# Performance work log

Hardware: AMD Instinct MI355X
Metric: run time of the kernel (lower is better)

Reference implementation:

```python
import jax, jax.numpy as jnp
import numpy as np

DIM = 32
B, H, W = 4, 256, 256


def conv1x1(x, w, b):
    # x: [B,C,H,W], w: [O,C], b: [O]
    return jnp.einsum('bchw,oc->bohw', x, w) + b[None, :, None, None]


def conv3x3(x, w, b):
    # x: [B,C,H,W], w: [O,C,3,3]
    out = jax.lax.conv_general_dilated(
        x, w, window_strides=(1, 1), padding='SAME',
        dimension_numbers=('NCHW', 'OIHW', 'NCHW'))
    return out + b[None, :, None, None]


def fft2d(x):
    # fft2 over last two dims, then fftshift over ALL dims (torch default)
    f = jnp.fft.fftshift(jnp.fft.fft2(x, norm='ortho'))
    return jnp.concatenate([f.real, f.imag], axis=1)  # [B,2C,H,W]


def ifft2d(x):
    f = jnp.fft.ifftshift(x)  # over ALL dims (torch default)
    re, im = jnp.split(f, 2, axis=1)
    c = jax.lax.complex(re, im)
    return jnp.abs(jnp.fft.ifft2(c, norm='ortho'))  # [B,C,H,W]


def setup_inputs() -> dict:
    key = jax.random.key(0)
    ks = jax.random.split(key, 16)
    C = DIM
    s = 0.02  # small init keeps the global-HW dot products in a sane softmax range
    inp = {
        'x': jax.random.normal(ks[0], (B, C, H, W), jnp.float32),
        'y': jax.random.normal(ks[1], (B, C, H, W), jnp.float32),
        'wq': jax.random.normal(ks[2], (C, C), jnp.float32) * s,
        'bq': jnp.zeros((C,), jnp.float32),
        'wk': jax.random.normal(ks[3], (C, C), jnp.float32) * s,
        'bk': jnp.zeros((C,), jnp.float32),
        'wv': jax.random.normal(ks[4], (C, C), jnp.float32) * s,
        'bv': jnp.zeros((C,), jnp.float32),
        'wd': jax.random.normal(ks[5], (C, C), jnp.float32) * s,
        'bd': jnp.zeros((C,), jnp.float32),
        'wc': jax.random.normal(ks[6], (2 * C, 2 * C, 3, 3), jnp.float32) * s,
        'bc': jnp.zeros((2 * C,), jnp.float32),
        'wi': jax.random.normal(ks[7], (2 * C, 2 * C, 3, 3), jnp.float32) * s,
        'bi': jnp.zeros((2 * C,), jnp.float32),
    }
    return inp


def reference(x, y, wq, bq, wk, bk, wv, bv, wd, bd, wc, bc, wi, bi):
    b, c, h, w = x.shape
    xq = conv1x1(x, wq, bq).reshape(b, c, h * w)            # [B,C,HW]
    dft = conv3x3(fft2d(conv1x1(y, wd, bd)), wc, bc)        # [B,2C,H,W]
    yk, yv = jnp.split(dft, 2, axis=1)
    yk = conv1x1(yk, wk, bk).reshape(b, c, h * w)
    yv = conv1x1(yv, wv, bv).reshape(b, c, h * w)
    att = jnp.einsum('bcn,bdn->bcd', xq, yk)                # [B,C,C]
    att = jax.nn.softmax(att, axis=1)                       # softmax over dim=1 (as in torch)
    out = jnp.einsum('bcd,bdn->bcn', att, yv).reshape(b, c, h, w)
    out = out + ifft2d(conv3x3(jax.nn.relu(dft), wi, bi))
    return out
```

## Files before the change

### kernel.cpp

```cpp
#include <hip/hip_runtime.h>
#include <math.h>

#define HW_ (256*256)
#define CH 32
#define CH2 64
#define BATCH 4

typedef short bf16x8 __attribute__((ext_vector_type(8)));
typedef float f32x4 __attribute__((ext_vector_type(4)));

__device__ __forceinline__ unsigned short f2bf(float f) {
    union { float f; unsigned u; } v; v.f = f;
    unsigned r = v.u + 0x7fffu + ((v.u >> 16) & 1u);
    return (unsigned short)(r >> 16);
}
__device__ __forceinline__ float bf2f(unsigned h) {
    union { unsigned u; float f; } v; v.u = h << 16;
    return v.f;
}

__device__ __forceinline__ int ctof_slot(int s) {
    return s < 16 ? s + 16 : s < 32 ? s + 32 : s < 48 ? s - 32 : s - 16;
}

__device__ __forceinline__ float2 cmul(float2 a, float2 b) {
    return make_float2(a.x*b.x - a.y*b.y, a.x*b.y + a.y*b.x);
}

__device__ __forceinline__ uint4 relu_bf16x8(uint4 v) {
    unsigned* pv = (unsigned*)&v;
    #pragma unroll
    for (int q = 0; q < 4; ++q) {
        unsigned a = pv[q];
        unsigned lo = a & 0xffffu, hi = a >> 16;
        if (lo & 0x8000u) lo = 0;
        if (hi & 0x8000u) hi = 0;
        pv[q] = lo | (hi << 16);
    }
    return v;
}

__device__ __forceinline__ void build_tw4(float2* tw, float sign) {
    int tid = threadIdx.x;
    float ang = sign * 6.2831853071795864769f * (float)tid / 256.0f;
    float s, c; sincosf(ang, &s, &c);
    tw[tid] = make_float2(c, s);
}

template<int SGN>
__device__ __forceinline__ void fft16_reg(float2* x, const float2* tw) {
    float2 u[16];
    #pragma unroll
    for (int m0 = 0; m0 < 4; ++m0) {
        float2 x0 = x[m0], x1 = x[m0+4], x2 = x[m0+8], x3 = x[m0+12];
        float2 t0 = make_float2(x0.x+x2.x, x0.y+x2.y);
        float2 t1 = make_float2(x0.x-x2.x, x0.y-x2.y);
        float2 t2 = make_float2(x1.x+x3.x, x1.y+x3.y);
        float2 t3 = make_float2(x1.x-x3.x, x1.y-x3.y);
        float2 r  = make_float2(-SGN*t3.y, SGN*t3.x);
        u[m0*4+0] = make_float2(t0.x+t2.x, t0.y+t2.y);
        u[m0*4+1] = make_float2(t1.x+r.x,  t1.y+r.y);
        u[m0*4+2] = make_float2(t0.x-t2.x, t0.y-t2.y);
        u[m0*4+3] = make_float2(t1.x-r.x,  t1.y-r.y);
    }
    #pragma unroll
    for (int m0 = 1; m0 < 4; ++m0)
        #pragma unroll
        for (int a = 1; a < 4; ++a)
            u[m0*4+a] = cmul(u[m0*4+a], tw[(16*m0*a) & 255]);
    #pragma unroll
    for (int a = 0; a < 4; ++a) {
        float2 x0 = u[a], x1 = u[4+a], x2 = u[8+a], x3 = u[12+a];
        float2 t0 = make_float2(x0.x+x2.x, x0.y+x2.y);
        float2 t1 = make_float2(x0.x-x2.x, x0.y-x2.y);
        float2 t2 = make_float2(x1.x+x3.x, x1.y+x3.y);
        float2 t3 = make_float2(x1.x-x3.x, x1.y-x3.y);
        float2 r  = make_float2(-SGN*t3.y, SGN*t3.x);
        x[a]    = make_float2(t0.x+t2.x, t0.y+t2.y);
        x[a+4]  = make_float2(t1.x+r.x,  t1.y+r.y);
        x[a+8]  = make_float2(t0.x-t2.x, t0.y-t2.y);
        x[a+12] = make_float2(t1.x-r.x,  t1.y-r.y);
    }
}

template<int SGN>
__device__ __forceinline__ void fft_core16(float2* A, const float2* tw) {
    const int tid = threadIdx.x;
    const int l = tid >> 4;
    const int d = tid & 15;
    const int base = l*257;
    float2 x[16];
    #pragma unroll
    for (int n1 = 0; n1 < 16; ++n1) x[n1] = A[base + n1*16 + d];
    fft16_reg<SGN>(x, tw);
    #pragma unroll
    for (int k0 = 1; k0 < 16; ++k0) x[k0] = cmul(x[k0], tw[d*k0]);
    #pragma unroll
    for (int k0 = 0; k0 < 16; ++k0) A[base + k0*16 + ((d + k0) & 15)] = x[k0];
    __syncthreads();
    #pragma unroll
    for (int n0 = 0; n0 < 16; ++n0) x[n0] = A[base + d*16 + ((n0 + d) & 15)];
    fft16_reg<SGN>(x, tw);
    #pragma unroll
    for (int k1 = 0; k1 < 16; ++k1) A[base + d + k1*16] = x[k1];
    __syncthreads();
}

__global__ __launch_bounds__(256) void k_fft_fwd1(const unsigned short* __restrict__ yd, ushort2* __restrict__ CAt) {
    __shared__ float2 A[16*257];
    __shared__ float2 tw[256];
    build_tw4(tw, -1.0f);
    int blk = blockIdx.x;
    int bc = blk >> 4, h0 = (blk & 15) << 4;
    const float sc = 1.0f/16.0f;
    const unsigned short* src = yd + (size_t)bc*HW_ + (size_t)h0*256;
    for (int idx = threadIdx.x; idx < 16*64; idx += 256) {
        int l = idx >> 6, w4 = (idx & 63) << 2;
        uint2 v = *(const uint2*)(src + l*256 + w4);
        A[l*257 + w4+0] = make_float2(bf2f(v.x & 0xffffu)*sc, 0.0f);
        A[l*257 + w4+1] = make_float2(bf2f(v.x >> 16)*sc, 0.0f);
        A[l*257 + w4+2] = make_float2(bf2f(v.y & 0xffffu)*sc, 0.0f);
        A[l*257 + w4+3] = make_float2(bf2f(v.y >> 16)*sc, 0.0f);
    }
    __syncthreads();
    fft_core16<-1>(A, tw);
    int t = threadIdx.x;
    unsigned short pk[32];
    #pragma unroll
    for (int l = 0; l < 16; ++l) {
        float2 v = A[l*257 + t];
        pk[2*l]   = f2bf(v.x);
        pk[2*l+1] = f2bf(v.y);
    }
    uint4* d4 = (uint4*)(CAt + (size_t)bc*HW_ + (size_t)t*256 + h0);
    const uint4* s4 = (const uint4*)pk;
    d4[0] = s4[0]; d4[1] = s4[1]; d4[2] = s4[2]; d4[3] = s4[3];
}

__global__ __launch_bounds__(256) void k_fft_fwd2(const ushort2* __restrict__ CAt, unsigned short* __restrict__ FSH) {
    __shared__ float2 A[16*257];
    __shared__ float2 tw[256];
    build_tw4(tw, -1.0f);
    int blk = blockIdx.x;
    int b = blk >> 9, chalf = (blk >> 8) & 1, w = blk & 255;
    const float sc = 1.0f/16.0f;
    const ushort2* src = CAt + (((size_t)(b*32 + chalf*16))*256 + w)*256;
    for (int idx = threadIdx.x; idx < 16*256; idx += 256) {
        int l = idx >> 8, h = idx & 255;
        ushort2 v = src[(size_t)l*HW_ + h];
        A[l*257 + h] = make_float2(bf2f(v.x)*sc, bf2f(v.y)*sc);
    }
    __syncthreads();
    fft_core16<-1>(A, tw);
    int t = threadIdx.x;
    int bt = (b + 2) & 3;
    int ht = (t + 128) & 255;
    int wt = (w + 128) & 255;
    unsigned short pk[32];
    #pragma unroll
    for (int l = 0; l < 16; ++l) {
        float2 v = A[l*257 + t];
        pk[l]      = f2bf(v.x);
        pk[16 + l] = f2bf(v.y);
    }
    unsigned short* dst = FSH + ((((size_t)bt*256 + ht)*256 + wt)*64 + chalf*32);
    uint4* d4 = (uint4*)dst;
    const uint4* s4 = (const uint4*)pk;
    d4[0] = s4[0]; d4[1] = s4[1]; d4[2] = s4[2]; d4[3] = s4[3];
}

__global__ __launch_bounds__(256) void k_conv1x1w(const float* __restrict__ in, const float* __restrict__ w,
                                                  const float* __restrict__ bias, unsigned short* __restrict__ out,
                                                  const float* __restrict__ wc, const float* __restrict__ wi,
                                                  unsigned short* __restrict__ d1, unsigned short* __restrict__ d2) {
    __shared__ float ts[32*257];
    int blk = blockIdx.x;
    int tid = threadIdx.x;
    if (blk >= 1024) {
        int i = (blk - 1024)*256 + tid;
        int half = i >= 36864;
        int j = i - half*36864;
        int tap = j >> 12, rem = j & 4095, oc = rem >> 6, s = rem & 63;
        if (half) {
            d2[j] = f2bf(wi[((size_t)(oc*64 + s))*9 + tap]);
        } else {
            int ic = ctof_slot(s);
            d1[j] = f2bf(wc[((size_t)(oc*64 + ic))*9 + tap]);
        }
        return;
    }
    int b = blk >> 8, h = blk & 255;
    const float* src = in + (size_t)b*CH*HW_ + (size_t)h*256;
    for (int idx = tid; idx < 32*256; idx += 256) {
        int c = idx >> 8, ww = idx & 255;
        ts[c*257 + ww] = src[(size_t)c*HW_ + ww];
    }
    __syncthreads();
    float acc[32];
    #pragma unroll
    for (int o = 0; o < 32; ++o) acc[o] = bias[o];
    for (int c = 0; c < 32; ++c) {
        float v = ts[c*257 + tid];
        #pragma unroll
        for (int o = 0; o < 32; ++o) acc[o] += w[o*32 + c] * v;
    }
    unsigned short* dst = out + (size_t)b*CH*HW_ + (size_t)h*256 + tid;
    #pragma unroll
    for (int o = 0; o < 32; ++o) dst[(size_t)o*HW_] = f2bf(acc[o]);
}

template<int MODE>
__global__ __launch_bounds__(256) void k_conv3(const unsigned short* __restrict__ in_cl,
                                               const unsigned short* __restrict__ wpk,
                                               const float* __restrict__ bias,
                                               unsigned short* __restrict__ outp) {
    __shared__ __align__(16) char Xs[2112*16];
    __shared__ __align__(16) char Ws[1536*16];
    int tid = threadIdx.x;
    int blk = blockIdx.x;
    int wseg = blk & 3, hg = (blk >> 2) & 63, b = blk >> 8;
    int h0 = hg*4, w0 = wseg*64;

    const uint4* wsrc = (const uint4*)wpk;

    for (int gl = tid; gl < 2112; gl += 256) {
        int slot = gl / 528;
        int rem  = gl - slot*528;
        int col  = rem >> 3, hseg = rem & 7;
        int hh = h0 - 1 + slot;
        int wcol = w0 - 1 + col;
        uint4 v = make_uint4(0,0,0,0);
        if (hh >= 0 && hh < 256 && wcol >= 0 && wcol < 256) {
            v = *(const uint4*)(in_cl + (((size_t)(b*256 + hh)*256 + wcol)*64) + hseg*8);
            if (MODE == 1) v = relu_bf16x8(v);
        }
        *(uint4*)(Xs + ((gl << 4) ^ ((col & 7) << 4))) = v;
    }
    #pragma unroll
    for (int q = 0; q < 6; ++q) {
        int gw = tid + q*256;
        int oc = (gw >> 3) & 63;
        *(uint4*)(Ws + ((gw << 4) ^ ((oc & 7) << 4))) = wsrc[gw];
    }
    __syncthreads();

    int lane = tid & 63;
    int wv = tid >> 6;
    int l16 = lane & 15, lq = lane >> 4;

    f32x4 acc[4][4];
    #pragma unroll
    for (int i = 0; i < 4; ++i)
        #pragma unroll
        for (int j = 0; j < 4; ++j) acc[i][j] = (f32x4)0.0f;

    for (int dy = 0; dy < 3; ++dy) {
        uint4 xr0 = make_uint4(0,0,0,0), xr1 = make_uint4(0,0,0,0), xr2 = make_uint4(0,0,0,0);
        uint4 wr[6];
        if (dy < 2) {
            int hh = h0 + dy + 2;
            bool hv = hh < 256;
            {
                int gl = tid;
                int col = gl >> 3, hseg = gl & 7;
                int wcol = w0 - 1 + col;
                if (hv && wcol >= 0 && wcol < 256)
                    xr0 = *(const uint4*)(in_cl + (((size_t)(b*256 + hh)*256 + wcol)*64) + hseg*8);
            }
            {
                int gl = tid + 256;
                int col = gl >> 3, hseg = gl & 7;
                int wcol = w0 - 1 + col;
                if (hv && wcol >= 0 && wcol < 256)
                    xr1 = *(const uint4*)(in_cl + (((size_t)(b*256 + hh)*256 + wcol)*64) + hseg*8);
            }
            if (tid < 16) {
                int gl = tid + 512;
                int col = gl >> 3, hseg = gl & 7;
                int wcol = w0 - 1 + col;
                if (hv && wcol < 256)
                    xr2 = *(const uint4*)(in_cl + (((size_t)(b*256 + hh)*256 + wcol)*64) + hseg*8);
            }
            #pragma unroll
            for (int q = 0; q < 6; ++q)
                wr[q] = wsrc[(dy+1)*1536 + tid + q*256];
        }

        int slot = (wv + dy) & 3;
        #pragma unroll
        for (int dx = 0; dx < 3; ++dx) {
            #pragma unroll
            for (int kk = 0; kk < 2; ++kk) {
                int hseg = kk*4 + lq;
                bf16x8 xf[4], wf[4];
                #pragma unroll
                for (int j = 0; j < 4; ++j) {
                    int col = j*16 + l16 + dx;
                    int g = slot*528 + col*8 + hseg;
                    xf[j] = *(const bf16x8*)(Xs + ((g << 4) ^ ((col & 7) << 4)));
                }
                #pragma unroll
                for (int i = 0; i < 4; ++i) {
                    int oc = i*16 + l16;
                    int lw = dx*512 + oc*8 + hseg;
                    wf[i] = *(const bf16x8*)(Ws + ((lw << 4) ^ ((oc & 7) << 4)));
                    #pragma unroll
                    for (int j = 0; j < 4; ++j) {
                        if (MODE == 0)
                            acc[i][j] = __builtin_amdgcn_mfma_f32_16x16x32_bf16(wf[i], xf[j], acc[i][j], 0, 0, 0);
                        else
                            acc[i][j] = __builtin_amdgcn_mfma_f32_16x16x32_bf16(xf[j], wf[i], acc[i][j], 0, 0, 0);
                    }
                }
            }
        }

        if (dy < 2) {
            __syncthreads();
            int slotn = (dy + 3) & 3;
            {
                int gl = tid;
                int col = gl >> 3;
                uint4 v = (MODE == 1) ? relu_bf16x8(xr0) : xr0;
                int g = slotn*528 + gl;
                *(uint4*)(Xs + ((g << 4) ^ ((col & 7) << 4))) = v;
            }
            {
                int gl = tid + 256;
                int col = gl >> 3;
                uint4 v = (MODE == 1) ? relu_bf16x8(xr1) : xr1;
                int g = slotn*528 + gl;
                *(uint4*)(Xs + ((g << 4) ^ ((col & 7) << 4))) = v;
            }
            if (tid < 16) {
                int gl = tid + 512;
                int col = gl >> 3;
                uint4 v = (MODE == 1) ? relu_bf16x8(xr2) : xr2;
                int g = slotn*528 + gl;
                *(uint4*)(Xs + ((g << 4) ^ ((col & 7) << 4))) = v;
            }
            #pragma unroll
            for (int q = 0; q < 6; ++q) {
                int gw = tid + q*256;
                int oc = (gw >> 3) & 63;
                *(uint4*)(Ws + ((gw << 4) ^ ((oc & 7) << 4))) = wr[q];
            }
            __syncthreads();
        }
    }

    __syncthreads();
    char* Es = Xs;
    if (MODE == 0) {
        #pragma unroll
        for (int j = 0; j < 4; ++j) {
            int px = j*16 + l16;
            int rowswz = (px & 7) << 4;
            #pragma unroll
            for (int i = 0; i < 4; ++i) {
                int oc0 = i*16 + lq*4;
                float4 bv = *(const float4*)(bias + oc0);
                unsigned short c0 = f2bf(acc[i][j][0] + bv.x);
                unsigned short c1 = f2bf(acc[i][j][1] + bv.y);
                unsigned short c2 = f2bf(acc[i][j][2] + bv.z);
                unsigned short c3 = f2bf(acc[i][j][3] + bv.w);
                uint2 u;
                u.x = (unsigned)c0 | ((unsigned)c1 << 16);
                u.y = (unsigned)c2 | ((unsigned)c3 << 16);
                int byte = wv*8192 + px*128 + oc0*2;
                *(uint2*)(Es + (byte ^ rowswz)) = u;
            }
        }
    } else {
        #pragma unroll
        for (int i = 0; i < 4; ++i) {
            int oc = i*16 + l16;
            int rowswz = (oc & 7) << 4;
            float bv = bias[oc];
            #pragma unroll
            for (int j = 0; j < 4; ++j) {
                int px0 = j*16 + lq*4;
                unsigned short c0 = f2bf(acc[i][j][0] + bv);
                unsigned short c1 = f2bf(acc[i][j][1] + bv);
                unsigned short c2 = f2bf(acc[i][j][2] + bv);
                unsigned short c3 = f2bf(acc[i][j][3] + bv);
                uint2 u;
                u.x = (unsigned)c0 | ((unsigned)c1 << 16);
                u.y = (unsigned)c2 | ((unsigned)c3 << 16);
                int byte = wv*8192 + oc*128 + px0*2;
                *(uint2*)(Es + (byte ^ rowswz)) = u;
            }
        }
    }
    __syncthreads();
    #pragma unroll
    for (int q = 0; q < 8; ++q) {
        int off = (q*256 + tid)*16;
        uint4 v = *(const uint4*)(Es + (off ^ (((off >> 7) & 7) << 4)));
        int wvp = off >> 13;
        int row = (off >> 7) & 63;
        int bir = off & 127;
        if (MODE == 0) {
            *(uint4*)(outp + (((size_t)(b*256 + h0 + wvp)*256 + w0 + row)*64) + (bir >> 1)) = v;
        } else {
            *(uint4*)(outp + ((size_t)(b*64 + row)*HW_) + (size_t)(h0 + wvp)*256 + w0 + (bir >> 1)) = v;
        }
    }
}

__global__ __launch_bounds__(256) void k_gram(const float* __restrict__ x, const unsigned short* __restrict__ dcl,
                                              float* __restrict__ Mpart, float* __restrict__ Sxp, float* __restrict__ Sdp) {
    __shared__ __align__(16) float xs[32*132];
    __shared__ __align__(16) unsigned short dst_[32*136];
    __shared__ float mred[1024];
    __shared__ float sxred[32];
    __shared__ float sdred[32];
    int blk = blockIdx.x;
    int b = blk >> 7, chunk = blk & 127;
    int tid = threadIdx.x, lane = tid & 63, wv = tid >> 6;
    int l16 = lane & 15, lq = lane >> 4;
    for (int idx = tid; idx < 1024; idx += 256) mred[idx] = 0.0f;
    if (tid < 32) { sxred[tid] = 0.0f; sdred[tid] = 0.0f; }

    const float* xb = x + (size_t)b*CH*HW_;
    const unsigned short* db = dcl + (size_t)b*HW_*64;

    f32x4 acc[2][2];
    #pragma unroll
    for (int i = 0; i < 2; ++i)
        #pragma unroll
        for (int j = 0; j < 2; ++j) acc[i][j] = (f32x4)0.0f;
    float sx0 = 0, sx1 = 0, sd0 = 0, sd1 = 0;

    for (int q4 = 0; q4 < 4; ++q4) {
        int px0 = chunk*512 + q4*128;
        __syncthreads();
        #pragma unroll
        for (int p = 0; p < 4; ++p) {
            int g = tid + p*256;
            int c = g >> 5, k4 = (g & 31) << 2;
            *(float4*)&xs[c*132 + k4] = *(const float4*)(xb + (size_t)c*HW_ + px0 + k4);
        }
        #pragma unroll
        for (int p = 0; p < 2; ++p) {
            int g = tid + p*256;
            int px = g >> 2, quad = g & 3;
            uint4 v = *(const uint4*)(db + (size_t)(px0 + px)*64 + quad*8);
            const unsigned short* pv = (const unsigned short*)&v;
            #pragma unroll
            for (int u = 0; u < 8; ++u) dst_[(quad*8 + u)*136 + px] = pv[u];
        }
        __syncthreads();
        #pragma unroll
        for (int ks = 0; ks < 4; ++ks) {
            int k0 = ks*32 + lq*8;
            float4 xa = *(const float4*)&xs[l16*132 + k0];
            float4 xc = *(const float4*)&xs[l16*132 + k0 + 4];
            float4 ya = *(const float4*)&xs[(16+l16)*132 + k0];
            float4 yc = *(const float4*)&xs[(16+l16)*132 + k0 + 4];
            bf16x8 a0, a1;
            const float* pxa = (const float*)&xa;
            const float* pxc = (const float*)&xc;
            const float* pya = (const float*)&ya;
            const float* pyc = (const float*)&yc;
            #pragma unroll
            for (int j = 0; j < 4; ++j) {
                a0[j]   = (short)f2bf(pxa[j]);  sx0 += pxa[j];
                a0[4+j] = (short)f2bf(pxc[j]);  sx0 += pxc[j];
                a1[j]   = (short)f2bf(pya[j]);  sx1 += pya[j];
                a1[4+j] = (short)f2bf(pyc[j]);  sx1 += pyc[j];
            }
            bf16x8 b0 = *(const bf16x8*)&dst_[l16*136 + k0];
            bf16x8 b1 = *(const bf16x8*)&dst_[(16+l16)*136 + k0];
            #pragma unroll
            for (int j = 0; j < 8; ++j) {
                sd0 += bf2f((unsigned short)b0[j]);
                sd1 += bf2f((unsigned short)b1[j]);
            }
            acc[0][0] = __builtin_amdgcn_mfma_f32_16x16x32_bf16(a0, b0, acc[0][0], 0, 0, 0);
            acc[0][1] = __builtin_amdgcn_mfma_f32_16x16x32_bf16(a0, b1, acc[0][1], 0, 0, 0);
            acc[1][0] = __builtin_amdgcn_mfma_f32_16x16x32_bf16(a1, b0, acc[1][0], 0, 0, 0);
            acc[1][1] = __builtin_amdgcn_mfma_f32_16x16x32_bf16(a1, b1, acc[1][1], 0, 0, 0);
        }
    }
    __syncthreads();

    #pragma unroll
    for (int fi = 0; fi < 2; ++fi)
        #pragma unroll
        for (int fj = 0; fj < 2; ++fj)
            #pragma unroll
            for (int r = 0; r < 4; ++r)
                atomicAdd(&mred[(fi*16 + lq*4 + r)*32 + fj*16 + l16], acc[fi][fj][r]);

    sx0 += __shfl_xor(sx0, 16); sx0 += __shfl_xor(sx0, 32);
    sx1 += __shfl_xor(sx1, 16); sx1 += __shfl_xor(sx1, 32);
    sd0 += __shfl_xor(sd0, 16); sd0 += __shfl_xor(sd0, 32);
    sd1 += __shfl_xor(sd1, 16); sd1 += __shfl_xor(sd1, 32);
    if (lane < 16) {
        atomicAdd(&sxred[l16], sx0);
        atomicAdd(&sxred[l16 + 16], sx1);
        atomicAdd(&sdred[l16], sd0);
        atomicAdd(&sdred[l16 + 16], sd1);
    }
    __syncthreads();

    float* mp = Mpart + ((size_t)(b*128 + chunk))*1024;
    for (int idx = tid; idx < 1024; idx += 256) mp[idx] = mred[idx];
    if (tid < 32) {
        Sxp[(b*128 + chunk)*32 + tid] = sxred[tid];
        Sdp[(b*128 + chunk)*32 + tid] = sdred[tid];
    }
}

__global__ __launch_bounds__(256) void k_att(const float* __restrict__ Mpart, const float* __restrict__ Sxp,
                                              const float* __restrict__ Sdp,
                                              const float* __restrict__ wq, const float* __restrict__ bq,
                                              const float* __restrict__ wk, const float* __restrict__ bk,
                                              const float* __restrict__ wv, const float* __restrict__ bv,
                                              float* __restrict__ att2, float* __restrict__ sout) {
    __shared__ float Mls[1024], T1[1024], attls[32*33];
    __shared__ float wqs[1024], wks[1024], wvs[1024];
    __shared__ float q1[32], k1[32], sxs[32], sds[32];
    int tid = threadIdx.x;
    int b = blockIdx.x;
    for (int idx = tid; idx < 1024; idx += 256) { wqs[idx] = wq[idx]; wks[idx] = wk[idx]; wvs[idx] = wv[idx]; }
    #pragma unroll
    for (int q = 0; q < 4; ++q) {
        int o = tid + q*256;
        float s = 0;
        for (int c = 0; c < 128; ++c) s += Mpart[((size_t)(b*128 + c))*1024 + o];
        Mls[o] = s;
    }
    if (tid < 32) { float s = 0; for (int c = 0; c < 128; ++c) s += Sxp[(b*128 + c)*32 + tid]; sxs[tid] = s; }
    else if (tid < 64) { int e = tid - 32; float s = 0; for (int c = 0; c < 128; ++c) s += Sdp[(b*128 + c)*32 + e]; sds[e] = s; }
    __syncthreads();
    if (tid < 32) { float s=0; for (int a=0;a<32;++a) s += wqs[tid*32+a]*sxs[a]; q1[tid]=s; }
    else if (tid < 64) { int d=tid-32; float s=0; for (int e=0;e<32;++e) s += wks[d*32+e]*sds[e]; k1[d]=s; }
    for (int idx = tid; idx < 1024; idx += 256) {
        int c = idx >> 5, e = idx & 31;
        float s = 0;
        for (int a=0;a<32;++a) s += wqs[c*32+a]*Mls[a*32+e];
        T1[idx] = s;
    }
    __syncthreads();
    for (int idx = tid; idx < 1024; idx += 256) {
        int c = idx >> 5, d = idx & 31;
        float s = 0;
        for (int e=0;e<32;++e) s += T1[c*32+e]*wks[d*32+e];
        s += bq[c]*k1[d] + bk[d]*q1[c] + 65536.0f*bq[c]*bk[d];
        attls[c*33+d] = s;
    }
    __syncthreads();
    if (tid < 32) {
        int d = tid;
        float mx = -1e30f;
        for (int c=0;c<32;++c) mx = fmaxf(mx, attls[c*33+d]);
        float sum = 0;
        for (int c=0;c<32;++c) { float e_ = expf(attls[c*33+d]-mx); attls[c*33+d]=e_; sum+=e_; }
        float inv = 1.0f/sum;
        for (int c=0;c<32;++c) attls[c*33+d] *= inv;
    }
    __syncthreads();
    for (int idx = tid; idx < 1024; idx += 256) {
        int c = idx >> 5, e = idx & 31;
        float s = 0;
        for (int d=0; d<32; ++d) s += attls[c*33+d]*wvs[d*32+e];
        att2[b*1024 + idx] = s;
    }
    if (tid < 32) {
        float s=0; for (int d=0;d<32;++d) s += attls[tid*33+d]*bv[d];
        sout[b*32+tid] = s;
    }
}

__global__ __launch_bounds__(256) void k_fft_inv1(const unsigned short* __restrict__ G, ushort2* __restrict__ Z1T) {
    __shared__ float2 A[16*257];
    __shared__ float2 tw[256];
    build_tw4(tw, 1.0f);
    int blk = blockIdx.x;
    int bc = blk >> 4, w0 = (blk & 15) << 4;
    int b = bc >> 5, c = bc & 31;
    int bs = (b + 2) & 3;
    const float sc = 1.0f/16.0f;
    const unsigned short* gre = G + ((size_t)(bs*CH2 + c + 32))*HW_;
    const unsigned short* gim = G + ((size_t)(bs*CH2 + c))*HW_;
    for (int idx = threadIdx.x; idx < 16*256; idx += 256) {
        int h = idx >> 4, l = idx & 15;
        int hs = (h + 128) & 255;
        int ws = (w0 + l + 128) & 255;
        A[l*257 + h] = make_float2(bf2f(gre[(size_t)hs*256 + ws])*sc, bf2f(gim[(size_t)hs*256 + ws])*sc);
    }
    __syncthreads();
    fft_core16<1>(A, tw);
    ushort2* dst = Z1T + (size_t)bc*HW_;
    for (int idx = threadIdx.x; idx < 16*256; idx += 256) {
        int l = idx >> 8, h = idx & 255;
        float2 v = A[l*257 + h];
        dst[(size_t)(w0 + l)*256 + h] = make_ushort2(f2bf(v.x), f2bf(v.y));
    }
}

__global__ __launch_bounds__(256) void k_fft_inv2(const ushort2* __restrict__ Z1T, unsigned short* __restrict__ Mag) {
    __shared__ float2 A[16*257];
    __shared__ float2 tw[256];
    build_tw4(tw, 1.0f);
    int blk = blockIdx.x;
    int bc = blk >> 4, h0 = (blk & 15) << 4;
    const float sc = 1.0f/16.0f;
    const ushort2* src = Z1T + (size_t)bc*HW_ + h0;
    for (int idx = threadIdx.x; idx < 16*256; idx += 256) {
        int w = idx >> 4, l = idx & 15;
        ushort2 v = src[(size_t)w*256 + l];
        A[l*257 + w] = make_float2(bf2f(v.x)*sc, bf2f(v.y)*sc);
    }
    __syncthreads();
    fft_core16<1>(A, tw);
    unsigned short* dst = Mag + (size_t)bc*HW_ + (size_t)h0*256;
    for (int idx = threadIdx.x; idx < 16*256; idx += 256) {
        int l = idx >> 8, w = idx & 255;
        float2 v = A[l*257 + w];
        dst[l*256 + w] = f2bf(sqrtf(v.x*v.x + v.y*v.y));
    }
}

__global__ __launch_bounds__(256) void k_out(const unsigned short* __restrict__ dcl, const float* __restrict__ att2,
                                             const float* __restrict__ sv, const unsigned short* __restrict__ Mag,
                                             float* __restrict__ out) {
    __shared__ __align__(16) float A2ls[1024];
    __shared__ float svls[32];
    int blk = blockIdx.x; int b = blk >> 8, h = blk & 255;
    int tid = threadIdx.x;
    for (int idx = tid; idx < 1024; idx += 256) A2ls[idx] = att2[b*1024 + idx];
    if (tid < 32) svls[tid] = sv[b*32 + tid];
    __syncthreads();
    int px = tid;
    const uint4* dvp = (const uint4*)(dcl + ((((size_t)b*256 + h)*256 + px)*64 + 32));
    uint4 d0 = dvp[0], d1 = dvp[1];
    unsigned u[8] = {d0.x, d0.y, d0.z, d0.w, d1.x, d1.y, d1.z, d1.w};
    float dv[32];
    #pragma unroll
    for (int i = 0; i < 8; ++i) {
        dv[2*i]   = bf2f(u[i] & 0xffffu);
        dv[2*i+1] = bf2f(u[i] >> 16);
    }
    float accv[32];
    #pragma unroll
    for (int c = 0; c < 32; ++c) accv[c] = svls[c];
    #pragma unroll
    for (int q = 0; q < 8; ++q) {
        #pragma unroll
        for (int c = 0; c < 32; ++c) {
            float4 a4 = *(const float4*)&A2ls[c*32 + q*4];
            accv[c] += a4.x*dv[q*4] + a4.y*dv[q*4+1] + a4.z*dv[q*4+2] + a4.w*dv[q*4+3];
        }
    }
    const unsigned short* mb = Mag + (size_t)b*CH*HW_ + (size_t)h*256 + px;
    float* ob = out + (size_t)b*CH*HW_ + (size_t)h*256 + px;
    #pragma unroll
    for (int c = 0; c < 32; ++c) ob[(size_t)c*HW_] = accv[c] + bf2f(mb[(size_t)c*HW_]);
}

extern "C" void kernel_launch(void* const* d_in, const int* in_sizes, int n_in,
                              void* d_out, int out_size, void* d_ws, size_t ws_size,
                              hipStream_t stream) {
    const float* x  = (const float*)d_in[0];
    const float* y  = (const float*)d_in[1];
    const float* wq = (const float*)d_in[2];
    const float* bq = (const float*)d_in[3];
    const float* wk = (const float*)d_in[4];
    const float* bk = (const float*)d_in[5];
    const float* wv = (const float*)d_in[6];
    const float* bv = (const float*)d_in[7];
    const float* wd = (const float*)d_in[8];
    const float* bd = (const float*)d_in[9];
    const float* wc = (const float*)d_in[10];
    const float* bc = (const float*)d_in[11];
    const float* wi = (const float*)d_in[12];
    const float* bi = (const float*)d_in[13];
    float* out = (float*)d_out;

    char* ws = (char*)d_ws;
    size_t o = 0;
    unsigned short* R1   = (unsigned short*)(ws + o); o += (size_t)BATCH*CH*HW_*2;
    ushort2*        CAt  = (ushort2*)(ws + o);        o += (size_t)BATCH*CH*HW_*4;
    unsigned short* FSHc = (unsigned short*)(ws + o); o += (size_t)BATCH*CH2*HW_*2;
    unsigned short* DFTc = (unsigned short*)(ws + o); o += (size_t)BATCH*CH2*HW_*2;
    unsigned short* Gpl  = (unsigned short*)(ws + o); o += (size_t)BATCH*CH2*HW_*2;
    unsigned short* wpk1 = (unsigned short*)(ws + o); o += 9*64*64*2;
    unsigned short* wpk2 = (unsigned short*)(ws + o); o += 9*64*64*2;
    float*          Mpart= (float*)(ws + o);          o += (size_t)512*1024*4;
    float*          Sxp  = (float*)(ws + o);          o += 512*32*4;
    float*          Sdp  = (float*)(ws + o);          o += 512*32*4;
    float*          A2b  = (float*)(ws + o);          o += 4096*4;
    float*          Svb  = (float*)(ws + o);          o += 128*4;
    if (ws_size < o) return;

    ushort2*        Z1T = CAt;
    unsigned short* Mag = R1;

    k_conv1x1w<<<1312, 256, 0, stream>>>(y, wd, bd, R1, wc, wi, wpk1, wpk2);
    k_fft_fwd1<<<2048, 256, 0, stream>>>(R1, CAt);
    k_fft_fwd2<<<2048, 256, 0, stream>>>(CAt, FSHc);
    k_conv3<0><<<1024, 256, 0, stream>>>(FSHc, wpk1, bc, DFTc);
    k_conv3<1><<<1024, 256, 0, stream>>>(DFTc, wpk2, bi, Gpl);
    k_gram<<<512, 256, 0, stream>>>(x, DFTc, Mpart, Sxp, Sdp);
    k_att<<<4, 256, 0, stream>>>(Mpart, Sxp, Sdp, wq, bq, wk, bk, wv, bv, A2b, Svb);
    k_fft_inv1<<<2048, 256, 0, stream>>>(Gpl, Z1T);
    k_fft_inv2<<<2048, 256, 0, stream>>>(Z1T, Mag);
    k_out<<<1024, 256, 0, stream>>>(DFTc, A2b, Svb, Mag, out);
}
```

Before: 275.5 us.

## Pack channel pairs into complex FFT and stream conv3 weights from global

```diff
diff --git a/kernel.cpp b/kernel.cpp
--- a/kernel.cpp
+++ b/kernel.cpp
@@ -111,16 +111,19 @@
     __shared__ float2 tw[256];
     build_tw4(tw, -1.0f);
     int blk = blockIdx.x;
-    int bc = blk >> 4, h0 = (blk & 15) << 4;
+    int bp = blk >> 4, h0 = (blk & 15) << 4;
+    int b = bp >> 4, p = bp & 15;
     const float sc = 1.0f/16.0f;
-    const unsigned short* src = yd + (size_t)bc*HW_ + (size_t)h0*256;
+    const unsigned short* s0 = yd + ((size_t)(b*CH + 2*p))*HW_ + (size_t)h0*256;
+    const unsigned short* s1 = s0 + HW_;
     for (int idx = threadIdx.x; idx < 16*64; idx += 256) {
         int l = idx >> 6, w4 = (idx & 63) << 2;
-        uint2 v = *(const uint2*)(src + l*256 + w4);
-        A[l*257 + w4+0] = make_float2(bf2f(v.x & 0xffffu)*sc, 0.0f);
-        A[l*257 + w4+1] = make_float2(bf2f(v.x >> 16)*sc, 0.0f);
-        A[l*257 + w4+2] = make_float2(bf2f(v.y & 0xffffu)*sc, 0.0f);
-        A[l*257 + w4+3] = make_float2(bf2f(v.y >> 16)*sc, 0.0f);
+        uint2 va = *(const uint2*)(s0 + l*256 + w4);
+        uint2 vb = *(const uint2*)(s1 + l*256 + w4);
+        A[l*257 + w4+0] = make_float2(bf2f(va.x & 0xffffu)*sc, bf2f(vb.x & 0xffffu)*sc);
+        A[l*257 + w4+1] = make_float2(bf2f(va.x >> 16)*sc, bf2f(vb.x >> 16)*sc);
+        A[l*257 + w4+2] = make_float2(bf2f(va.y & 0xffffu)*sc, bf2f(vb.y & 0xffffu)*sc);
+        A[l*257 + w4+3] = make_float2(bf2f(va.y >> 16)*sc, bf2f(vb.y >> 16)*sc);
     }
     __syncthreads();
     fft_core16<-1>(A, tw);
@@ -132,7 +135,7 @@
         pk[2*l]   = f2bf(v.x);
         pk[2*l+1] = f2bf(v.y);
     }
-    uint4* d4 = (uint4*)(CAt + (size_t)bc*HW_ + (size_t)t*256 + h0);
+    uint4* d4 = (uint4*)(CAt + (size_t)bp*HW_ + (size_t)t*256 + h0);
     const uint4* s4 = (const uint4*)pk;
     d4[0] = s4[0]; d4[1] = s4[1]; d4[2] = s4[2]; d4[3] = s4[3];
 }
@@ -142,12 +145,15 @@
     __shared__ float2 tw[256];
     build_tw4(tw, -1.0f);
     int blk = blockIdx.x;
-    int b = blk >> 9, chalf = (blk >> 8) & 1, w = blk & 255;
+    int b = blk >> 8, ph = (blk >> 7) & 1, vu = blk & 127;
+    bool sp = (vu == 0);
+    int col0 = vu, col1 = sp ? 128 : (256 - vu);
     const float sc = 1.0f/16.0f;
-    const ushort2* src = CAt + (((size_t)(b*32 + chalf*16))*256 + w)*256;
     for (int idx = threadIdx.x; idx < 16*256; idx += 256) {
         int l = idx >> 8, h = idx & 255;
-        ushort2 v = src[(size_t)l*HW_ + h];
+        int p = l >> 1, s = l & 1;
+        int col = s ? col1 : col0;
+        ushort2 v = CAt[((size_t)(b*16 + ph*8 + p)*256 + col)*256 + h];
         A[l*257 + h] = make_float2(bf2f(v.x)*sc, bf2f(v.y)*sc);
     }
     __syncthreads();
@@ -155,18 +161,31 @@
     int t = threadIdx.x;
     int bt = (b + 2) & 3;
     int ht = (t + 128) & 255;
-    int wt = (w + 128) & 255;
-    unsigned short pk[32];
-    #pragma unroll
-    for (int l = 0; l < 16; ++l) {
-        float2 v = A[l*257 + t];
-        pk[l]      = f2bf(v.x);
-        pk[16 + l] = f2bf(v.y);
-    }
-    unsigned short* dst = FSH + ((((size_t)bt*256 + ht)*256 + wt)*64 + chalf*32);
-    uint4* d4 = (uint4*)dst;
-    const uint4* s4 = (const uint4*)pk;
-    d4[0] = s4[0]; d4[1] = s4[1]; d4[2] = s4[2]; d4[3] = s4[3];
+    int tn = (256 - t) & 255;
+    #pragma unroll
+    for (int s = 0; s < 2; ++s) {
+        int v = s ? col1 : col0;
+        int wt = (v + 128) & 255;
+        unsigned short pk[32];
+        #pragma unroll
+        for (int p = 0; p < 8; ++p) {
+            int lA = 2*p + s;
+            int lB = sp ? lA : (2*p + 1 - s);
+            float2 Za = A[lA*257 + t];
+            float2 Zb = A[lB*257 + tn];
+            float xr = (Za.x + Zb.x)*0.5f, xi = (Za.y - Zb.y)*0.5f;
+            float dr = Za.x - Zb.x,        di = Za.y + Zb.y;
+            float yr = di*0.5f,            yi = -dr*0.5f;
+            pk[2*p]     = f2bf(xr);
+            pk[2*p+1]   = f2bf(yr);
+            pk[16+2*p]  = f2bf(xi);
+            pk[17+2*p]  = f2bf(yi);
+        }
+        unsigned short* dst = FSH + ((((size_t)bt*256 + ht)*256 + wt)*64 + ph*32);
+        uint4* d4 = (uint4*)dst;
+        const uint4* s4 = (const uint4*)pk;
+        d4[0] = s4[0]; d4[1] = s4[1]; d4[2] = s4[2]; d4[3] = s4[3];
+    }
 }
 
 __global__ __launch_bounds__(256) void k_conv1x1w(const float* __restrict__ in, const float* __restrict__ w,
@@ -215,13 +234,14 @@
                                                const float* __restrict__ bias,
                                                unsigned short* __restrict__ outp) {
     __shared__ __align__(16) char Xs[2112*16];
-    __shared__ __align__(16) char Ws[1536*16];
     int tid = threadIdx.x;
     int blk = blockIdx.x;
     int wseg = blk & 3, hg = (blk >> 2) & 63, b = blk >> 8;
     int h0 = hg*4, w0 = wseg*64;
 
-    const uint4* wsrc = (const uint4*)wpk;
+    int lane = tid & 63;
+    int wv = tid >> 6;
+    int l16 = lane & 15, lq = lane >> 4;
 
     for (int gl = tid; gl < 2112; gl += 256) {
         int slot = gl / 528;
@@ -236,17 +256,16 @@
         }
         *(uint4*)(Xs + ((gl << 4) ^ ((col & 7) << 4))) = v;
     }
-    #pragma unroll
-    for (int q = 0; q < 6; ++q) {
-        int gw = tid + q*256;
-        int oc = (gw >> 3) & 63;
-        *(uint4*)(Ws + ((gw << 4) ^ ((oc & 7) << 4))) = wsrc[gw];
-    }
-    __syncthreads();
-
-    int lane = tid & 63;
-    int wv = tid >> 6;
-    int l16 = lane & 15, lq = lane >> 4;
+
+    const unsigned short* wb = wpk + ((size_t)((lane & 15) + ((tid & 32) ? 0 : 0)))*0;
+    bf16x8 wcur[8], wnxt[8];
+    #pragma unroll
+    for (int q = 0; q < 8; ++q) {
+        int oc = (q >> 1)*16 + l16;
+        int hs = (q & 1)*4 + lq;
+        wcur[q] = *(const bf16x8*)(wpk + oc*64 + hs*8);
+    }
+    __syncthreads();
 
     f32x4 acc[4][4];
     #pragma unroll
@@ -254,108 +273,104 @@
         #pragma unroll
         for (int j = 0; j < 4; ++j) acc[i][j] = (f32x4)0.0f;
 
-    for (int dy = 0; dy < 3; ++dy) {
-        uint4 xr0 = make_uint4(0,0,0,0), xr1 = make_uint4(0,0,0,0), xr2 = make_uint4(0,0,0,0);
-        uint4 wr[6];
-        if (dy < 2) {
-            int hh = h0 + dy + 2;
+    uint4 xr0 = make_uint4(0,0,0,0), xr1 = make_uint4(0,0,0,0), xr2 = make_uint4(0,0,0,0);
+
+    #pragma unroll
+    for (int tap = 0; tap < 9; ++tap) {
+        const int dy = tap / 3, dx = tap - dy*3;
+
+        if (tap < 8) {
+            #pragma unroll
+            for (int q = 0; q < 8; ++q) {
+                int oc = (q >> 1)*16 + l16;
+                int hs = (q & 1)*4 + lq;
+                wnxt[q] = *(const bf16x8*)(wpk + (size_t)(tap+1)*4096 + oc*64 + hs*8);
+            }
+        }
+        if (dx == 0 && dy < 2) {
+            int hh = h0 + dy + 3;
             bool hv = hh < 256;
+            xr0 = make_uint4(0,0,0,0); xr1 = make_uint4(0,0,0,0); xr2 = make_uint4(0,0,0,0);
             {
-                int gl = tid;
-                int col = gl >> 3, hseg = gl & 7;
+                int gl = tid; int col = gl >> 3, hs = gl & 7;
                 int wcol = w0 - 1 + col;
                 if (hv && wcol >= 0 && wcol < 256)
-                    xr0 = *(const uint4*)(in_cl + (((size_t)(b*256 + hh)*256 + wcol)*64) + hseg*8);
+                    xr0 = *(const uint4*)(in_cl + (((size_t)(b*256 + hh)*256 + wcol)*64) + hs*8);
             }
             {
-                int gl = tid + 256;
-                int col = gl >> 3, hseg = gl & 7;
+                int gl = tid + 256; int col = gl >> 3, hs = gl & 7;
                 int wcol = w0 - 1 + col;
                 if (hv && wcol >= 0 && wcol < 256)
-                    xr1 = *(const uint4*)(in_cl + (((size_t)(b*256 + hh)*256 + wcol)*64) + hseg*8);
+                    xr1 = *(const uint4*)(in_cl + (((size_t)(b*256 + hh)*256 + wcol)*64) + hs*8);
             }
             if (tid < 16) {
-                int gl = tid + 512;
-                int col = gl >> 3, hseg = gl & 7;
+                int gl = tid + 512; int col = gl >> 3, hs = gl & 7;
                 int wcol = w0 - 1 + col;
                 if (hv && wcol < 256)
-                    xr2 = *(const uint4*)(in_cl + (((size_t)(b*256 + hh)*256 + wcol)*64) + hseg*8);
-            }
-            #pragma unroll
-            for (int q = 0; q < 6; ++q)
-                wr[q] = wsrc[(dy+1)*1536 + tid + q*256];
+                    xr2 = *(const uint4*)(in_cl + (((size_t)(b*256 + hh)*256 + wcol)*64) + hs*8);
+            }
         }
 
         int slot = (wv + dy) & 3;
         #pragma unroll
-        for (int dx = 0; dx < 3; ++dx) {
-            #pragma unroll
-            for (int kk = 0; kk < 2; ++kk) {
-                int hseg = kk*4 + lq;
-                bf16x8 xf[4], wf[4];
+        for (int kk = 0; kk < 2; ++kk) {
+            int hs = kk*4 + lq;
+            bf16x8 xf[4];
+            #pragma unroll
+            for (int j = 0; j < 4; ++j) {
+                int col = j*16 + l16 + dx;
+                int g = slot*528 + col*8 + hs;
+                xf[j] = *(const bf16x8*)(Xs + ((g << 4) ^ ((col & 7) << 4)));
+            }
+            #pragma unroll
+            for (int i = 0; i < 4; ++i) {
+                bf16x8 wf = wcur[i*2 + kk];
                 #pragma unroll
                 for (int j = 0; j < 4; ++j) {
-                    int col = j*16 + l16 + dx;
-                    int g = slot*528 + col*8 + hseg;
-                    xf[j] = *(const bf16x8*)(Xs + ((g << 4) ^ ((col & 7) << 4)));
+                    if (MODE == 0)
+                        acc[i][j] = __builtin_amdgcn_mfma_f32_16x16x32_bf16(wf, xf[j], acc[i][j], 0, 0, 0);
+                    else
+                        acc[i][j] = __builtin_amdgcn_mfma_f32_16x16x32_bf16(xf[j], wf, acc[i][j], 0, 0, 0);
                 }
-                #pragma unroll
-                for (int i = 0; i < 4; ++i) {
-                    int oc = i*16 + l16;
-                    int lw = dx*512 + oc*8 + hseg;
-                    wf[i] = *(const bf16x8*)(Ws + ((lw << 4) ^ ((oc & 7) << 4)));
-                    #pragma unroll
-                    for (int j = 0; j < 4; ++j) {
-                        if (MODE == 0)
-                            acc[i][j] = __builtin_amdgcn_mfma_f32_16x16x32_bf16(wf[i], xf[j], acc[i][j], 0, 0, 0);
-                        else
-                            acc[i][j] = __builtin_amdgcn_mfma_f32_16x16x32_bf16(xf[j], wf[i], acc[i][j], 0, 0, 0);
-                    }
-                }
-            }
-        }
-
-        if (dy < 2) {
+            }
+        }
+
+        if (dx == 2 && dy < 2) {
             __syncthreads();
-            int slotn = (dy + 3) & 3;
+            int slotn = dy & 3;
             {
-                int gl = tid;
-                int col = gl >> 3;
+                int gl = tid; int col = gl >> 3;
                 uint4 v = (MODE == 1) ? relu_bf16x8(xr0) : xr0;
                 int g = slotn*528 + gl;
                 *(uint4*)(Xs + ((g << 4) ^ ((col & 7) << 4))) = v;
             }
             {
-                int gl = tid + 256;
-                int col = gl >> 3;
+                int gl = tid + 256; int col = gl >> 3;
                 uint4 v = (MODE == 1) ? relu_bf16x8(xr1) : xr1;
                 int g = slotn*528 + gl;
                 *(uint4*)(Xs + ((g << 4) ^ ((col & 7) << 4))) = v;
             }
             if (tid < 16) {
-                int gl = tid + 512;
-                int col = gl >> 3;
+                int gl = tid + 512; int col = gl >> 3;
                 uint4 v = (MODE == 1) ? relu_bf16x8(xr2) : xr2;
                 int g = slotn*528 + gl;
                 *(uint4*)(Xs + ((g << 4) ^ ((col & 7) << 4))) = v;
             }
-            #pragma unroll
-            for (int q = 0; q < 6; ++q) {
-                int gw = tid + q*256;
-                int oc = (gw >> 3) & 63;
-                *(uint4*)(Ws + ((gw << 4) ^ ((oc & 7) << 4))) = wr[q];
-            }
             __syncthreads();
         }
-    }
-
-    __syncthreads();
-    char* Es = Xs;
+
+        if (tap < 8) {
+            #pragma unroll
+            for (int q = 0; q < 8; ++q) wcur[q] = wnxt[q];
+        }
+    }
+
+    int h = h0 + wv;
     if (MODE == 0) {
         #pragma unroll
         for (int j = 0; j < 4; ++j) {
-            int px = j*16 + l16;
-            int rowswz = (px & 7) << 4;
+            int px = w0 + j*16 + l16;
+            unsigned short* orow = outp + (((size_t)b*256 + h)*256 + px)*64;
             #pragma unroll
             for (int i = 0; i < 4; ++i) {
                 int oc0 = i*16 + lq*4;
@@ -367,19 +382,18 @@
                 uint2 u;
                 u.x = (unsigned)c0 | ((unsigned)c1 << 16);
                 u.y = (unsigned)c2 | ((unsigned)c3 << 16);
-                int byte = wv*8192 + px*128 + oc0*2;
-                *(uint2*)(Es + (byte ^ rowswz)) = u;
+                *(uint2*)(orow + oc0) = u;
             }
         }
     } else {
         #pragma unroll
         for (int i = 0; i < 4; ++i) {
             int oc = i*16 + l16;
-            int rowswz = (oc & 7) << 4;
             float bv = bias[oc];
+            unsigned short* oplane = outp + ((size_t)b*64 + oc)*HW_ + (size_t)h*256;
             #pragma unroll
             for (int j = 0; j < 4; ++j) {
-                int px0 = j*16 + lq*4;
+                int px0 = w0 + j*16 + lq*4;
                 unsigned short c0 = f2bf(acc[i][j][0] + bv);
                 unsigned short c1 = f2bf(acc[i][j][1] + bv);
                 unsigned short c2 = f2bf(acc[i][j][2] + bv);
@@ -387,23 +401,8 @@
                 uint2 u;
                 u.x = (unsigned)c0 | ((unsigned)c1 << 16);
                 u.y = (unsigned)c2 | ((unsigned)c3 << 16);
-                int byte = wv*8192 + oc*128 + px0*2;
-                *(uint2*)(Es + (byte ^ rowswz)) = u;
-            }
-        }
-    }
-    __syncthreads();
-    #pragma unroll
-    for (int q = 0; q < 8; ++q) {
-        int off = (q*256 + tid)*16;
-        uint4 v = *(const uint4*)(Es + (off ^ (((off >> 7) & 7) << 4)));
-        int wvp = off >> 13;
-        int row = (off >> 7) & 63;
-        int bir = off & 127;
-        if (MODE == 0) {
-            *(uint4*)(outp + (((size_t)(b*256 + h0 + wvp)*256 + w0 + row)*64) + (bir >> 1)) = v;
-        } else {
-            *(uint4*)(outp + ((size_t)(b*64 + row)*HW_) + (size_t)(h0 + wvp)*256 + w0 + (bir >> 1)) = v;
+                *(uint2*)(oplane + px0) = u;
+            }
         }
     }
 }
@@ -700,8 +699,8 @@
     unsigned short* Mag = R1;
 
     k_conv1x1w<<<1312, 256, 0, stream>>>(y, wd, bd, R1, wc, wi, wpk1, wpk2);
-    k_fft_fwd1<<<2048, 256, 0, stream>>>(R1, CAt);
-    k_fft_fwd2<<<2048, 256, 0, stream>>>(CAt, FSHc);
+    k_fft_fwd1<<<1024, 256, 0, stream>>>(R1, CAt);
+    k_fft_fwd2<<<1024, 256, 0, stream>>>(CAt, FSHc);
     k_conv3<0><<<1024, 256, 0, stream>>>(FSHc, wpk1, bc, DFTc);
     k_conv3<1><<<1024, 256, 0, stream>>>(DFTc, wpk2, bi, Gpl);
     k_gram<<<512, 256, 0, stream>>>(x, DFTc, Mpart, Sxp, Sdp);
```

After: 291.6 us. 5.9% more time.
